# Performance work log

Measured on AMD Instinct MI355X. Metric: run time of the kernel, lower is better.

Reference implementation:

```python
import jax, jax.numpy as jnp
import numpy as np

C = 256; CM = 8; MAXI = 100; NCLS = 80
KP = (CM + 2) * CM + CM + CM * CM + CM + CM + 1  # 169 dynamic-kernel params

def _ln(x, g, b, eps=1e-5):
    m = x.mean(-1, keepdims=True)
    v = ((x - m) ** 2).mean(-1, keepdims=True)
    return g * (x - m) * jax.lax.rsqrt(v + eps) + b

def _mlp(x, hw, hb, lng, lnb, fw, fb):
    # torchvision MLP: [Linear -> LayerNorm -> SiLU] * n_hidden -> Linear
    for i in range(hw.shape[0]):
        x = jax.nn.silu(_ln(x @ hw[i] + hb[i], lng[i], lnb[i]))
    return x @ fw + fb

def _conv1x1_bn(x, w, s, b):
    # 1x1 conv (no bias) + inference-mode BatchNorm folded into per-channel affine
    y = jnp.einsum('bchw,oc->bohw', x, w)
    return y * s[None, :, None, None] + b[None, :, None, None]

def _grid(h, w):
    # normalized cell-center coordinates, (x, y) order, shape [h, w, 2]
    ys = (jnp.arange(h, dtype=jnp.float32) + 0.5) / h
    xs = (jnp.arange(w, dtype=jnp.float32) + 0.5) / w
    return jnp.stack([jnp.broadcast_to(xs[None, :], (h, w)),
                      jnp.broadcast_to(ys[:, None], (h, w))], axis=-1)

def setup_inputs() -> dict:
    key = jax.random.key(0)
    ks = iter(jax.random.split(key, 40))
    nrm = lambda shape, s=0.02: s * jax.random.normal(next(ks), shape, jnp.float32)
    B = 4
    inp = {
        'x0': jax.random.normal(next(ks), (B, 3, 512, 512), jnp.float32),
        'x1': jax.random.normal(next(ks), (B, 64, 256, 256), jnp.float32),
        'x2': jax.random.normal(next(ks), (B, 128, 128, 128), jnp.float32),
        'x3': jax.random.normal(next(ks), (B, 256, 64, 64), jnp.float32),
        'x4': jax.random.normal(next(ks), (B, 512, 32, 32), jnp.float32),
        'x5': jax.random.normal(next(ks), (B, 1024, 16, 16), jnp.float32),
        'lat3_w': nrm((C, 256)), 'lat3_s': jnp.ones((C,)), 'lat3_b': jnp.zeros((C,)),
        'lat4_w': nrm((C, 512)), 'lat4_s': jnp.ones((C,)), 'lat4_b': jnp.zeros((C,)),
        'lat5_w': nrm((C, 1024)), 'lat5_s': jnp.ones((C,)), 'lat5_b': jnp.zeros((C,)),
        'mlat_w': nrm((C, 256)), 'mlat_s': jnp.ones((C,)), 'mlat_b': jnp.zeros((C,)),
        'mhead_w': nrm((CM, C, 3, 3)), 'mhead_s': jnp.ones((CM,)), 'mhead_b': jnp.zeros((CM,)),
        'loc_hw': nrm((4, C, C)), 'loc_hb': jnp.zeros((4, C)), 'loc_lng': jnp.ones((4, C)), 'loc_lnb': jnp.zeros((4, C)),
        'loc_fw': nrm((C, 1)), 'loc_fb': -5.0 * jnp.ones((1,)),
        'cls_hw': nrm((4, C, C)), 'cls_hb': jnp.zeros((4, C)), 'cls_lng': jnp.ones((4, C)), 'cls_lnb': jnp.zeros((4, C)),
        'cls_fw': nrm((C, NCLS)), 'cls_fb': jnp.zeros((NCLS,)),
        'ker_hw': nrm((4, C, C)), 'ker_hb': jnp.zeros((4, C)), 'ker_lng': jnp.ones((4, C)), 'ker_lnb': jnp.zeros((4, C)),
        'ker_fw': nrm((C, KP)), 'ker_fb': jnp.zeros((KP,)),
    }
    return inp

def reference(x0, x1, x2, x3, x4, x5,
              lat3_w, lat3_s, lat3_b, lat4_w, lat4_s, lat4_b, lat5_w, lat5_s, lat5_b,
              mlat_w, mlat_s, mlat_b, mhead_w, mhead_s, mhead_b,
              loc_hw, loc_hb, loc_lng, loc_lnb, loc_fw, loc_fb,
              cls_hw, cls_hb, cls_lng, cls_lnb, cls_fw, cls_fb,
              ker_hw, ker_hb, ker_lng, ker_lnb, ker_fw, ker_fb):
    B, _, H, W = x0.shape
    lvls = [(x3, lat3_w, lat3_s, lat3_b), (x4, lat4_w, lat4_s, lat4_b), (x5, lat5_w, lat5_s, lat5_b)]
    feats = [_conv1x1_bn(x, w, s, b) for (x, w, s, b) in lvls]
    flat = jnp.concatenate([f.reshape(B, C, -1).transpose(0, 2, 1) for f in feats], axis=1)  # [B, L, C]
    loc_logits = _mlp(flat, loc_hw, loc_hb, loc_lng, loc_lnb, loc_fw, loc_fb)[..., 0]       # [B, L]
    top_vals, top_idx = jax.lax.top_k(loc_logits, MAXI)
    scores = jax.nn.sigmoid(top_vals)
    num_instances = (scores > 0.5).sum(axis=1)
    gfeat = jnp.take_along_axis(flat, top_idx[:, :, None], axis=1)  # [B, I, C]
    # mask branch
    mf = _conv1x1_bn(x3, mlat_w, mlat_s, mlat_b)
    mf = jax.lax.conv_general_dilated(mf, mhead_w, (1, 1), 'SAME', dimension_numbers=('NCHW', 'OIHW', 'NCHW'))
    mf = jax.nn.silu(mf * mhead_s[None, :, None, None] + mhead_b[None, :, None, None])  # [B, CM, h3, w3]
    h3, w3 = x3.shape[2], x3.shape[3]
    offs_flat = jnp.concatenate([_grid(x.shape[2], x.shape[3]).reshape(-1, 2) for x in (x3, x4, x5)], axis=0)
    offs = offs_flat[top_idx]                                # [B, I, 2]
    grid = _grid(h3, w3).transpose(2, 0, 1)                  # [2, h3, w3]
    grid = grid[None, None] - offs[:, :, :, None, None]      # [B, I, 2, h, w]
    mfi = jnp.broadcast_to(mf[:, None], (B, MAXI, CM, h3, w3))
    feats_i = jnp.concatenate([mfi, grid], axis=2)           # [B, I, CM+2, h, w]
    dyn = _mlp(gfeat, ker_hw, ker_hb, ker_lng, ker_lnb, ker_fw, ker_fb)  # [B, I, KP]
    c = CM
    o = (c + 2) * c
    w1 = dyn[..., :o].reshape(B, MAXI, c + 2, c)
    b1 = dyn[..., o:o + c].reshape(B, MAXI, c, 1, 1); o += c
    w2 = dyn[..., o:o + c * c].reshape(B, MAXI, c, c); o += c * c
    b2 = dyn[..., o:o + c].reshape(B, MAXI, c, 1, 1); o += c
    w3 = dyn[..., o:o + c].reshape(B, MAXI, c, 1); o += c
    b3 = dyn[..., o:].reshape(B, MAXI, 1, 1, 1)
    m = jax.nn.silu(jnp.einsum('bichw,bicd->bidhw', feats_i, w1) + b1)
    m = jax.nn.silu(jnp.einsum('bichw,bicd->bidhw', m, w2) + b2)
    m = jnp.einsum('bichw,bicd->bidhw', m, w3) + b3
    masks = jax.nn.sigmoid(m[:, :, 0])                       # [B, I, h3, w3]
    classes = jnp.argmax(_mlp(gfeat, cls_hw, cls_hb, cls_lng, cls_lnb, cls_fw, cls_fb), axis=-1)
    masks = jax.image.resize(masks, (B, MAXI, H, W), method='bilinear', antialias=False)
    return (num_instances, scores, classes, masks)
```

## Files before the change

kernel.cpp:

```cpp
#include <hip/hip_runtime.h>
#include <hip/hip_bf16.h>
#include <math.h>

#define DEVI __device__ __forceinline__

constexpr int LTOT  = 5376;
constexpr int NINST = 100;
constexpr int NCLS  = 80;
constexpr int KPAR  = 169;

DEVI float waveAllSum(float v) {
#pragma unroll
  for (int s = 32; s > 0; s >>= 1) v += __shfl_xor(v, s, 64);
  return v;
}
DEVI float siluf(float x) { return x / (1.0f + expf(-x)); }
DEVI float sigmf(float x) { return 1.0f / (1.0f + expf(-x)); }

__global__ __launch_bounds__(256) void wtrans(
    const float* __restrict__ w3, const float* __restrict__ w4,
    const float* __restrict__ w5, const float* __restrict__ wm,
    float* __restrict__ wt3, float* __restrict__ wt4,
    float* __restrict__ wt5, float* __restrict__ wtm)
{
  __shared__ float t[64][65];
  const int bid = blockIdx.x;
  const float* src; float* dst; int K, rel;
  if (bid < 16)       { src = w3; dst = wt3; K = 256;  rel = bid; }
  else if (bid < 48)  { src = w4; dst = wt4; K = 512;  rel = bid - 16; }
  else if (bid < 112) { src = w5; dst = wt5; K = 1024; rel = bid - 48; }
  else                { src = wm; dst = wtm; K = 256;  rel = bid - 112; }
  const int ctiles = K >> 6;
  const int ot = rel / ctiles, ct = rel % ctiles;
  const int o0 = ot * 64, c0 = ct * 64;
  const int tid = threadIdx.x;
#pragma unroll
  for (int s = 0; s < 16; ++s) {
    const int e = tid + 256*s;
    const int r = e >> 6, c = e & 63;
    t[r][c] = src[(long)(o0 + r)*K + c0 + c];
  }
  __syncthreads();
#pragma unroll
  for (int s = 0; s < 16; ++s) {
    const int e = tid + 256*s;
    const int q = e >> 6, p = e & 63;
    dst[(long)(c0 + q)*256 + o0 + p] = t[p][q];
  }
}

__global__ __launch_bounds__(256) void lateral_main(
    const float* __restrict__ x3, const float* __restrict__ x4, const float* __restrict__ x5,
    const float* __restrict__ wt3, const float* __restrict__ s3, const float* __restrict__ b3,
    const float* __restrict__ wt4, const float* __restrict__ s4, const float* __restrict__ b4,
    const float* __restrict__ wt5, const float* __restrict__ s5, const float* __restrict__ b5,
    const float* __restrict__ wtm, const float* __restrict__ sm, const float* __restrict__ bm,
    float* __restrict__ flat, float* __restrict__ mlatb)
{
  __shared__ float xs[32][36];
  __shared__ float ws[32][256];
  const int tid = threadIdx.x;
  const int rg = tid >> 6, cg = tid & 63;
  const int bid = blockIdx.x;
  const float *x, *wt, *sc, *bi;
  int K, P, b, p0, baseL = 0; bool tomlat = false;
  if (bid < 512)       { x=x3; wt=wt3; sc=s3; bi=b3; K=256;  P=4096; b=bid>>7;  p0=(bid&127)*32; }
  else if (bid < 1024) { const int rel=bid-512;  x=x3; wt=wtm; sc=sm; bi=bm; K=256;  P=4096; b=rel>>7; p0=(rel&127)*32; tomlat=true; }
  else if (bid < 1152) { const int rel=bid-1024; x=x4; wt=wt4; sc=s4; bi=b4; K=512;  P=1024; b=rel>>5; p0=(rel&31)*32; baseL=4096; }
  else                 { const int rel=bid-1152; x=x5; wt=wt5; sc=s5; bi=b5; K=1024; P=256;  b=rel>>3; p0=(rel&7)*32;  baseL=5120; }
  const float* xb = x + (long)b * K * P;
  float acc[8][4] = {};
  const int nkb = K >> 5;
  for (int kb = 0; kb < nkb; ++kb) {
    __syncthreads();
#pragma unroll
    for (int s = 0; s < 4; ++s) {
      const int e = tid + 256*s;
      const int kk = e >> 5, px = e & 31;
      xs[kk][px] = xb[(long)(kb*32 + kk)*P + p0 + px];
    }
    {
      const float4* w4p = reinterpret_cast<const float4*>(wt + (kb << 13));
#pragma unroll
      for (int q = 0; q < 8; ++q) {
        const int c = tid + (q << 8);
        *reinterpret_cast<float4*>(&ws[c >> 6][4*(c & 63)]) = w4p[c];
      }
    }
    __syncthreads();
#pragma unroll
    for (int kk = 0; kk < 32; ++kk) {
      const float4 a0 = *reinterpret_cast<const float4*>(&xs[kk][8*rg]);
      const float4 a1 = *reinterpret_cast<const float4*>(&xs[kk][8*rg+4]);
      const float ar[8] = {a0.x,a0.y,a0.z,a0.w,a1.x,a1.y,a1.z,a1.w};
      const float4 wv = *reinterpret_cast<const float4*>(&ws[kk][4*cg]);
#pragma unroll
      for (int i = 0; i < 8; ++i) {
        acc[i][0] += ar[i]*wv.x; acc[i][1] += ar[i]*wv.y;
        acc[i][2] += ar[i]*wv.z; acc[i][3] += ar[i]*wv.w;
      }
    }
  }
  const float4 sA = *reinterpret_cast<const float4*>(&sc[4*cg]);
  const float4 bA = *reinterpret_cast<const float4*>(&bi[4*cg]);
  if (!tomlat) {
#pragma unroll
    for (int i = 0; i < 8; ++i) {
      const float4 ov = { acc[i][0]*sA.x+bA.x, acc[i][1]*sA.y+bA.y,
                          acc[i][2]*sA.z+bA.z, acc[i][3]*sA.w+bA.w };
      *reinterpret_cast<float4*>(&flat[((long)b*LTOT + baseL + p0 + 8*rg + i)*256 + 4*cg]) = ov;
    }
  } else {
#pragma unroll
    for (int j = 0; j < 4; ++j) {
      const float sj = (&sA.x)[j], bj = (&bA.x)[j];
      const float4 o0 = { acc[0][j]*sj+bj, acc[1][j]*sj+bj, acc[2][j]*sj+bj, acc[3][j]*sj+bj };
      const float4 o1 = { acc[4][j]*sj+bj, acc[5][j]*sj+bj, acc[6][j]*sj+bj, acc[7][j]*sj+bj };
      float* mb = &mlatb[((long)b*256 + 4*cg + j)*4096 + p0 + 8*rg];
      *reinterpret_cast<float4*>(mb) = o0;
      *reinterpret_cast<float4*>(mb + 4) = o1;
    }
  }
}

__global__ __attribute__((amdgpu_waves_per_eu(3, 3))) __launch_bounds__(256)
void loc4(
    const float* __restrict__ in, const float* __restrict__ hw,
    const float* __restrict__ hb, const float* __restrict__ lng, const float* __restrict__ lnb,
    const float* __restrict__ fw, const float* __restrict__ fb, float* __restrict__ logits)
{
  __shared__ float xls[4][7][256];
  const int tid = threadIdx.x;
  const int rg = tid >> 6, cg = tid & 63;
  const int r0 = blockIdx.x * 28 + rg * 7;
  float* xw = &xls[rg][0][0];
#pragma unroll
  for (int i = 0; i < 7; ++i) {
    const float4 v = *reinterpret_cast<const float4*>(&in[(long)(r0 + i)*256 + 4*cg]);
    *reinterpret_cast<float4*>(&xw[i*256 + 4*cg]) = v;
  }
  const float4 fw4 = *reinterpret_cast<const float4*>(&fw[4*cg]);
  const float fbv = fb[0];

#define LOADG(W, A, g)                                                      \
  {                                                                         \
    const int kk4 = (g) << 2;                                               \
    W[0] = *reinterpret_cast<const float4*>(&w[(kk4 + 0) << 8]);            \
    W[1] = *reinterpret_cast<const float4*>(&w[(kk4 + 1) << 8]);            \
    W[2] = *reinterpret_cast<const float4*>(&w[(kk4 + 2) << 8]);            \
    W[3] = *reinterpret_cast<const float4*>(&w[(kk4 + 3) << 8]);            \
    _Pragma("unroll")                                                       \
    for (int r = 0; r < 7; ++r)                                             \
      A[r] = *reinterpret_cast<const float4*>(&xw[r*256 + kk4]);            \
  }
#define FMAG(W, A)                                                          \
  _Pragma("unroll")                                                         \
  for (int u = 0; u < 4; ++u) {                                             \
    _Pragma("unroll")                                                       \
    for (int r = 0; r < 7; ++r) {                                           \
      const float a = (&A[r].x)[u];                                         \
      acc[r][0] += a*W[u].x; acc[r][1] += a*W[u].y;                         \
      acc[r][2] += a*W[u].z; acc[r][3] += a*W[u].w;                         \
    }                                                                       \
  }

  for (int L = 0; L < 4; ++L) {
    const float* w = hw + L*65536 + 4*cg;
    float acc[7][4] = {};
    float4 wvA[4], wvB[4], avA[7], avB[7];
    LOADG(wvA, avA, 0)
    for (int g = 0; g < 64; g += 2) {
      LOADG(wvB, avB, g + 1)
      FMAG(wvA, avA)
      if (g + 2 < 64) LOADG(wvA, avA, g + 2)
      FMAG(wvB, avB)
    }
    const float4 hb4 = *reinterpret_cast<const float4*>(&hb[L*256 + 4*cg]);
    const float4 g4  = *reinterpret_cast<const float4*>(&lng[L*256 + 4*cg]);
    const float4 lb4 = *reinterpret_cast<const float4*>(&lnb[L*256 + 4*cg]);
#pragma unroll
    for (int r = 0; r < 7; ++r) {
      const float y0 = acc[r][0]+hb4.x, y1 = acc[r][1]+hb4.y;
      const float y2 = acc[r][2]+hb4.z, y3 = acc[r][3]+hb4.w;
      const float m = waveAllSum(y0+y1+y2+y3) * (1.0f/256.0f);
      const float d0=y0-m, d1=y1-m, d2=y2-m, d3=y3-m;
      const float var = waveAllSum(d0*d0+d1*d1+d2*d2+d3*d3) * (1.0f/256.0f);
      const float rs = rsqrtf(var + 1e-5f);
      const float o0 = siluf(g4.x*d0*rs + lb4.x);
      const float o1 = siluf(g4.y*d1*rs + lb4.y);
      const float o2 = siluf(g4.z*d2*rs + lb4.z);
      const float o3 = siluf(g4.w*d3*rs + lb4.w);
      if (L < 3) {
        const float4 ov = {o0, o1, o2, o3};
        *reinterpret_cast<float4*>(&xw[r*256 + 4*cg]) = ov;
      } else {
        float d = o0*fw4.x + o1*fw4.y + o2*fw4.z + o3*fw4.w;
        d = waveAllSum(d);
        if (cg == 0) logits[r0 + r] = d + fbv;
      }
    }
  }
#undef LOADG
#undef FMAG
}

__global__ __launch_bounds__(256) void topk_gather(
    const float* __restrict__ logits, const float* __restrict__ flat,
    int* __restrict__ topi, float* __restrict__ gfeat,
    float* __restrict__ dout)
{
  __shared__ float sv[LTOT];
  __shared__ float rv[4];
  __shared__ int   ri[4];
  __shared__ int   sidx[NINST];
  const int b = blockIdx.x, tid = threadIdx.x;
  for (int l = tid; l < LTOT; l += 256) sv[l] = logits[b*LTOT + l];
  __syncthreads();
  int cnt = 0;
  for (int t = 0; t < NINST; ++t) {
    float bv = -INFINITY; int bidx = 0x7fffffff;
    for (int l = tid; l < LTOT; l += 256) {
      const float v = sv[l];
      if (v > bv) { bv = v; bidx = l; }
    }
#pragma unroll
    for (int s = 32; s > 0; s >>= 1) {
      const float v2 = __shfl_xor(bv, s, 64);
      const int   i2 = __shfl_xor(bidx, s, 64);
      if (v2 > bv || (v2 == bv && i2 < bidx)) { bv = v2; bidx = i2; }
    }
    if ((tid & 63) == 0) { rv[tid >> 6] = bv; ri[tid >> 6] = bidx; }
    __syncthreads();
    if (tid == 0) {
      bv = rv[0]; bidx = ri[0];
#pragma unroll
      for (int q = 1; q < 4; ++q)
        if (rv[q] > bv || (rv[q] == bv && ri[q] < bidx)) { bv = rv[q]; bidx = ri[q]; }
      sidx[t] = bidx; topi[b*NINST + t] = bidx;
      dout[4 + b*NINST + t] = sigmf(bv);
      if (bv > 0.0f) ++cnt;
      sv[bidx] = -INFINITY;
    }
    __syncthreads();
  }
  if (tid == 0) dout[b] = (float)cnt;
  for (int t = 0; t < NINST; ++t) {
    const int ix = sidx[t];
    gfeat[((long)b*NINST + t)*256 + tid] = flat[((long)b*LTOT + ix)*256 + tid];
  }
}

__global__ __launch_bounds__(256) void clsker4(
    const float* __restrict__ gfeat, float* __restrict__ h2,
    const float* __restrict__ chw, const float* __restrict__ chb,
    const float* __restrict__ cg_, const float* __restrict__ cb_,
    const float* __restrict__ khw, const float* __restrict__ khb,
    const float* __restrict__ kg_, const float* __restrict__ kb_)
{
  __shared__ float xs[256][12];
  __shared__ float wsm[16][256];
  const int tid = threadIdx.x;
  const int rg = tid >> 6, cg = tid & 63;
  const bool ker = blockIdx.x >= 50;
  const int r0 = (ker ? (blockIdx.x - 50) : blockIdx.x) * 8;
  const int outr0 = r0 + (ker ? 400 : 0);
  const float* hw = ker ? khw : chw;
  const float* hb = ker ? khb : chb;
  const float* g_ = ker ? kg_ : cg_;
  const float* lb = ker ? kb_ : cb_;
#pragma unroll
  for (int s = 0; s < 2; ++s) {
    const int e = tid + 256*s;
    const int row = e >> 6, q = e & 63;
    const float4 v = *reinterpret_cast<const float4*>(&gfeat[(long)(r0 + row)*256 + 4*q]);
    const int pc = 2*((row >> 1) ^ (q & 3)) + (row & 1);
#pragma unroll
    for (int j = 0; j < 4; ++j) xs[4*q+j][pc] = (&v.x)[j];
  }
  float ov[2][4];
  for (int L = 0; L < 4; ++L) {
    const float* w = hw + L*65536;
    float acc[2][4] = {};
    for (int kb = 0; kb < 16; ++kb) {
      __syncthreads();
      const float4* w4 = reinterpret_cast<const float4*>(w + (kb << 12));
#pragma unroll
      for (int q = 0; q < 4; ++q) {
        const int c = tid + (q << 8);
        *reinterpret_cast<float4*>(&wsm[c>>6][4*(c&63)]) = w4[c];
      }
      __syncthreads();
#pragma unroll
      for (int kk = 0; kk < 16; ++kk) {
        const int k = (kb << 4) + kk;
        const float2 av = *reinterpret_cast<const float2*>(&xs[k][2*(rg ^ ((k >> 2) & 3))]);
        const float4 wv = *reinterpret_cast<const float4*>(&wsm[kk][4*cg]);
        acc[0][0] += av.x*wv.x; acc[0][1] += av.x*wv.y; acc[0][2] += av.x*wv.z; acc[0][3] += av.x*wv.w;
        acc[1][0] += av.y*wv.x; acc[1][1] += av.y*wv.y; acc[1][2] += av.y*wv.z; acc[1][3] += av.y*wv.w;
      }
    }
    const float4 hb4 = *reinterpret_cast<const float4*>(&hb[L*256 + 4*cg]);
    const float4 g4  = *reinterpret_cast<const float4*>(&g_[L*256 + 4*cg]);
    const float4 lb4 = *reinterpret_cast<const float4*>(&lb[L*256 + 4*cg]);
#pragma unroll
    for (int i = 0; i < 2; ++i) {
      const float y0 = acc[i][0]+hb4.x, y1 = acc[i][1]+hb4.y;
      const float y2 = acc[i][2]+hb4.z, y3 = acc[i][3]+hb4.w;
      const float m = waveAllSum(y0+y1+y2+y3) * (1.0f/256.0f);
      const float d0=y0-m, d1=y1-m, d2=y2-m, d3=y3-m;
      const float var = waveAllSum(d0*d0+d1*d1+d2*d2+d3*d3) * (1.0f/256.0f);
      const float rs = rsqrtf(var + 1e-5f);
      ov[i][0] = siluf(g4.x*d0*rs + lb4.x);
      ov[i][1] = siluf(g4.y*d1*rs + lb4.y);
      ov[i][2] = siluf(g4.z*d2*rs + lb4.z);
      ov[i][3] = siluf(g4.w*d3*rs + lb4.w);
    }
    __syncthreads();
    if (L < 3) {
      const int pc = 2*(rg ^ (cg & 3));
#pragma unroll
      for (int j = 0; j < 4; ++j) {
        const float2 t = {ov[0][j], ov[1][j]};
        *reinterpret_cast<float2*>(&xs[4*cg+j][pc]) = t;
      }
    }
  }
#pragma unroll
  for (int i = 0; i < 2; ++i) {
    const float4 o = {ov[i][0], ov[i][1], ov[i][2], ov[i][3]};
    *reinterpret_cast<float4*>(&h2[(long)(outr0 + 2*rg + i)*256 + 4*cg]) = o;
  }
}

__global__ __launch_bounds__(256) void heads(
    const float* __restrict__ h2, const float* __restrict__ cfw, const float* __restrict__ cfb,
    const float* __restrict__ kfw, const float* __restrict__ kfb,
    float* __restrict__ dout, float* __restrict__ dyn)
{
  __shared__ float xr[256];
  __shared__ float lv[NCLS];
  const int bid = blockIdx.x, tid = threadIdx.x;
  xr[tid] = h2[(long)bid*256 + tid];
  __syncthreads();
  if (bid < 400) {
    if (tid < NCLS) {
      float a0=0.f, a1=0.f, a2=0.f, a3=0.f;
      for (int k = 0; k < 256; k += 4) {
        a0 += xr[k+0]*cfw[(k+0)*NCLS + tid];
        a1 += xr[k+1]*cfw[(k+1)*NCLS + tid];
        a2 += xr[k+2]*cfw[(k+2)*NCLS + tid];
        a3 += xr[k+3]*cfw[(k+3)*NCLS + tid];
      }
      lv[tid] = (a0+a1) + (a2+a3) + cfb[tid];
    }
    __syncthreads();
    if (tid == 0) {
      float bv = lv[0]; int bi2 = 0;
      for (int o = 1; o < NCLS; ++o) if (lv[o] > bv) { bv = lv[o]; bi2 = o; }
      dout[404 + bid] = (float)bi2;
    }
  } else {
    if (tid < KPAR) {
      float a0=0.f, a1=0.f, a2=0.f, a3=0.f;
      for (int k = 0; k < 256; k += 4) {
        a0 += xr[k+0]*kfw[(k+0)*KPAR + tid];
        a1 += xr[k+1]*kfw[(k+1)*KPAR + tid];
        a2 += xr[k+2]*kfw[(k+2)*KPAR + tid];
        a3 += xr[k+3]*kfw[(k+3)*KPAR + tid];
      }
      dyn[(long)(bid-400)*KPAR + tid] = (a0+a1) + (a2+a3) + kfb[tid];
    }
  }
}

__global__ __launch_bounds__(256) void conv3(
    const float* __restrict__ mlat, const float* __restrict__ mw,
    float* __restrict__ partial)
{
  const int bid = blockIdx.x;
  const int cc = bid & 7;
  const int tile = (bid >> 3) & 15;
  const int b = bid >> 7;
  const int y0 = (tile >> 2)*16, x0 = (tile & 3)*16;
  const int tid = threadIdx.x;
  const int ly = tid >> 4, lx = tid & 15;
  __shared__ float til[2][18][19];
  __shared__ float wch[8][32][12];
  for (int e = tid; e < 2304; e += 256) {
    const int o = e / 288, rem = e % 288;
    const int c = rem / 9, qq = rem - c*9;
    wch[o][c][qq] = mw[((o*256) + cc*32 + c)*9 + qq];
  }
  int lofs[3], gofs[3], chn[3]; bool vld[3], has[3];
  float* tf = &til[0][0][0];
#pragma unroll
  for (int s = 0; s < 3; ++s) {
    const int e = tid + 256*s;
    has[s] = (e < 648);
    lofs[s] = 0; gofs[s] = 0; chn[s] = 0; vld[s] = false;
    if (has[s]) {
      const int ch = (e >= 324) ? 1 : 0;
      const int pos = e - ch*324;
      const int iy = pos / 18, ix = pos - iy*18;
      const int gy = y0 - 1 + iy, gx = x0 - 1 + ix;
      vld[s] = (gy >= 0 && gy < 64 && gx >= 0 && gx < 64);
      lofs[s] = ch*342 + iy*19 + ix;
      gofs[s] = gy*64 + gx;
      chn[s] = ch;
    }
  }
  const float* xbase = mlat + ((long)b*256 + cc*32)*4096;
  float acc[8] = {};
  for (int r = 0; r < 16; ++r) {
    __syncthreads();
#pragma unroll
    for (int s = 0; s < 3; ++s)
      if (has[s]) tf[lofs[s]] = vld[s] ? xbase[(long)(2*r + chn[s])*4096 + gofs[s]] : 0.f;
    __syncthreads();
#pragma unroll
    for (int ch = 0; ch < 2; ++ch) {
      const int c = 2*r + ch;
      float t[9];
#pragma unroll
      for (int dy = 0; dy < 3; ++dy)
#pragma unroll
        for (int dx = 0; dx < 3; ++dx) t[dy*3+dx] = til[ch][ly+dy][lx+dx];
#pragma unroll
      for (int o = 0; o < 8; ++o) {
        const float4 wa = *reinterpret_cast<const float4*>(&wch[o][c][0]);
        const float4 wb = *reinterpret_cast<const float4*>(&wch[o][c][4]);
        const float w8 = wch[o][c][8];
        acc[o] += t[0]*wa.x + t[1]*wa.y + t[2]*wa.z + t[3]*wa.w
                + t[4]*wb.x + t[5]*wb.y + t[6]*wb.z + t[7]*wb.w + t[8]*w8;
      }
    }
  }
  const long pbase = (((long)b*8 + cc)*8)*4096 + (y0+ly)*64 + (x0+lx);
#pragma unroll
  for (int o = 0; o < 8; ++o) partial[pbase + (long)o*4096] = acc[o];
}

__global__ __launch_bounds__(256) void mhead_fin(
    const float* __restrict__ partial, const float* __restrict__ s,
    const float* __restrict__ bi, float* __restrict__ mhead)
{
  const int idx = blockIdx.x*256 + threadIdx.x;
  const int p = idx & 4095;
  const int o = (idx >> 12) & 7;
  const int b = idx >> 15;
  float v = 0.f;
#pragma unroll
  for (int cc = 0; cc < 8; ++cc) v += partial[(((long)b*8 + cc)*8 + o)*4096 + p];
  v = v*s[o] + bi[o];
  mhead[idx] = siluf(v);
}

__global__ __launch_bounds__(256) void mask_fused(
    const float* __restrict__ dyn, const int* __restrict__ topi,
    const float* __restrict__ mhead, float* __restrict__ dout)
{
  __shared__ float msrc[18][64];
  __shared__ float dd[KPAR];
  __shared__ float so[2];
  const int bid = blockIdx.x;
  const int inst = bid >> 2, q = bid & 3;
  const int tid = threadIdx.x;
  if (tid < KPAR) dd[tid] = dyn[(long)inst*KPAR + tid];
  if (tid == 0) {
    const int l = topi[inst];
    float ox, oy;
    if (l < 4096)      { ox = ((l & 63) + 0.5f)*(1.f/64.f); oy = ((l >> 6) + 0.5f)*(1.f/64.f); }
    else if (l < 5120) { const int t = l - 4096; ox = ((t & 31) + 0.5f)*(1.f/32.f); oy = ((t >> 5) + 0.5f)*(1.f/32.f); }
    else               { const int t = l - 5120; ox = ((t & 15) + 0.5f)*(1.f/16.f); oy = ((t >> 4) + 0.5f)*(1.f/16.f); }
    so[0] = ox; so[1] = oy;
  }
  __syncthreads();
  const float ox = so[0], oy = so[1];
  const int b = inst / NINST;
  const float* mh = mhead + (long)b*8*4096;
  const int r0s = 16*q - 1;
  for (int e = tid; e < 1152; e += 256) {
    const int r = e >> 6, x = e & 63;
    int sy = r0s + r; sy = sy < 0 ? 0 : (sy > 63 ? 63 : sy);
    const int p = sy*64 + x;
    float f[10];
#pragma unroll
    for (int c = 0; c < 8; ++c) f[c] = mh[c*4096 + p];
    f[8] = (x + 0.5f)*(1.f/64.f) - ox;
    f[9] = (sy + 0.5f)*(1.f/64.f) - oy;
    float m1[8];
#pragma unroll
    for (int d = 0; d < 8; ++d) {
      float t = dd[80 + d];
#pragma unroll
      for (int c = 0; c < 10; ++c) t += f[c]*dd[c*8 + d];
      m1[d] = siluf(t);
    }
    float m2[8];
#pragma unroll
    for (int d = 0; d < 8; ++d) {
      float t = dd[152 + d];
#pragma unroll
      for (int c = 0; c < 8; ++c) t += m1[c]*dd[88 + c*8 + d];
      m2[d] = siluf(t);
    }
    float o = dd[168];
#pragma unroll
    for (int c = 0; c < 8; ++c) o += m2[c]*dd[160 + c];
    msrc[r][x] = sigmf(o);
  }
  __syncthreads();
  const int j4 = tid & 127;
  const int half = tid >> 7;
  const int ix0 = (j4 & 1) ? (j4 >> 1) : (j4 >> 1) - 1;
  const int xlo = ix0 < 0 ? 0 : ix0;
  const int xhi = (ix0 + 1 > 63) ? 63 : ix0 + 1;
  float fx[4];
#pragma unroll
  for (int m = 0; m < 4; ++m) {
    const int x = 4*j4 + m;
    const float tx = (x + 0.5f)*0.125f - 0.5f;
    fx[m] = tx - (float)ix0;
  }
  float* dbase = dout + 804 + ((long)inst << 18);
  for (int it = 0; it < 64; ++it) {
    const int yy = 2*it + half;
    const int y = 128*q + yy;
    const float ty = (y + 0.5f)*0.125f - 0.5f;
    const float fyf = floorf(ty);
    const int iy0 = (int)fyf;
    const float fy = ty - fyf;
    const int r0 = iy0 - r0s;
    const float L0 = msrc[r0][xlo],   R0 = msrc[r0][xhi];
    const float L1 = msrc[r0+1][xlo], R1 = msrc[r0+1][xhi];
    const float L = L0 + (L1 - L0)*fy;
    const float R = R0 + (R1 - R0)*fy;
    const float4 ovv = { L + (R - L)*fx[0], L + (R - L)*fx[1],
                         L + (R - L)*fx[2], L + (R - L)*fx[3] };
    *reinterpret_cast<float4*>(&dbase[((long)y << 9) + (j4 << 2)]) = ovv;
  }
}

extern "C" void kernel_launch(void* const* d_in, const int* in_sizes, int n_in,
                              void* d_out, int out_size, void* d_ws, size_t ws_size,
                              hipStream_t stream)
{
  (void)in_sizes; (void)n_in; (void)out_size; (void)ws_size;
  const float* x3      = (const float*)d_in[3];
  const float* x4      = (const float*)d_in[4];
  const float* x5      = (const float*)d_in[5];
  const float* lat3_w  = (const float*)d_in[6];
  const float* lat3_s  = (const float*)d_in[7];
  const float* lat3_b  = (const float*)d_in[8];
  const float* lat4_w  = (const float*)d_in[9];
  const float* lat4_s  = (const float*)d_in[10];
  const float* lat4_b  = (const float*)d_in[11];
  const float* lat5_w  = (const float*)d_in[12];
  const float* lat5_s  = (const float*)d_in[13];
  const float* lat5_b  = (const float*)d_in[14];
  const float* mlat_w  = (const float*)d_in[15];
  const float* mlat_s  = (const float*)d_in[16];
  const float* mlat_b  = (const float*)d_in[17];
  const float* mhead_w = (const float*)d_in[18];
  const float* mhead_s = (const float*)d_in[19];
  const float* mhead_b = (const float*)d_in[20];
  const float* loc_hw  = (const float*)d_in[21];
  const float* loc_hb  = (const float*)d_in[22];
  const float* loc_lng = (const float*)d_in[23];
  const float* loc_lnb = (const float*)d_in[24];
  const float* loc_fw  = (const float*)d_in[25];
  const float* loc_fb  = (const float*)d_in[26];
  const float* cls_hw  = (const float*)d_in[27];
  const float* cls_hb  = (const float*)d_in[28];
  const float* cls_lng = (const float*)d_in[29];
  const float* cls_lnb = (const float*)d_in[30];
  const float* cls_fw  = (const float*)d_in[31];
  const float* cls_fb  = (const float*)d_in[32];
  const float* ker_hw  = (const float*)d_in[33];
  const float* ker_hb  = (const float*)d_in[34];
  const float* ker_lng = (const float*)d_in[35];
  const float* ker_lnb = (const float*)d_in[36];
  const float* ker_fw  = (const float*)d_in[37];
  const float* ker_fb  = (const float*)d_in[38];

  float* ws      = (float*)d_ws;
  float* flat    = ws;
  float* mlatb   = ws + 5505024;
  float* partial = ws + 9699328;
  float* mheadb  = ws + 10747904;
  float* h2      = ws + 10878976;
  float* logits  = ws + 11083776;
  int*   topi    = (int*)(ws + 11105280);
  float* gfeat   = ws + 11105680;
  float* dynb    = ws + 11208080;
  float* wt3     = ws + 11275680;
  float* wt4     = ws + 11341216;
  float* wt5     = ws + 11472288;
  float* wtm     = ws + 11734432;
  float* dout    = (float*)d_out;

  wtrans<<<128, 256, 0, stream>>>(lat3_w, lat4_w, lat5_w, mlat_w, wt3, wt4, wt5, wtm);
  lateral_main<<<1184, 256, 0, stream>>>(x3, x4, x5,
      wt3, lat3_s, lat3_b, wt4, lat4_s, lat4_b, wt5, lat5_s, lat5_b,
      wtm, mlat_s, mlat_b, flat, mlatb);
  conv3<<<512, 256, 0, stream>>>(mlatb, mhead_w, partial);
  mhead_fin<<<512, 256, 0, stream>>>(partial, mhead_s, mhead_b, mheadb);
  loc4<<<768, 256, 0, stream>>>(flat, loc_hw, loc_hb, loc_lng, loc_lnb,
                                loc_fw, loc_fb, logits);
  topk_gather<<<4, 256, 0, stream>>>(logits, flat, topi, gfeat, dout);
  clsker4<<<100, 256, 0, stream>>>(gfeat, h2,
      cls_hw, cls_hb, cls_lng, cls_lnb, ker_hw, ker_hb, ker_lng, ker_lnb);
  heads<<<800, 256, 0, stream>>>(h2, cls_fw, cls_fb, ker_fw, ker_fb, dout, dynb);
  mask_fused<<<1600, 256, 0, stream>>>(dynb, topi, mheadb, dout);
}
```

Baseline: 782.6 us.

## Cache per-thread top-k maxima and drop shared weight staging in hidden MLP

In top-k selection, each thread keeps its local best value and index and rescans its strided slice only when its candidate won the round. Previously every thread rescanned all of shared memory on each of the 100 iterations. The hidden-MLP kernel no longer stages weight tiles through shared memory behind block barriers. Each wave now streams weights directly from global memory with a software double-buffered register pipeline, and keeps its own two rows in a per-wave LDS slice. This removes most __syncthreads, at the cost of redundant global weight reads across the four waves, which rely on L1/L2 hits.

```diff
diff --git a/kernel.cpp b/kernel.cpp
--- a/kernel.cpp
+++ b/kernel.cpp
@@ -213,16 +213,18 @@
   __shared__ float rv[4];
   __shared__ int   ri[4];
   __shared__ int   sidx[NINST];
+  __shared__ int   winsh;
   const int b = blockIdx.x, tid = threadIdx.x;
   for (int l = tid; l < LTOT; l += 256) sv[l] = logits[b*LTOT + l];
   __syncthreads();
+  float bvt = -INFINITY; int bit = 0x7fffffff;
+  for (int l = tid; l < LTOT; l += 256) {
+    const float v = sv[l];
+    if (v > bvt) { bvt = v; bit = l; }
+  }
   int cnt = 0;
   for (int t = 0; t < NINST; ++t) {
-    float bv = -INFINITY; int bidx = 0x7fffffff;
-    for (int l = tid; l < LTOT; l += 256) {
-      const float v = sv[l];
-      if (v > bv) { bv = v; bidx = l; }
-    }
+    float bv = bvt; int bidx = bit;
 #pragma unroll
     for (int s = 32; s > 0; s >>= 1) {
       const float v2 = __shfl_xor(bv, s, 64);
@@ -239,11 +241,21 @@
       sidx[t] = bidx; topi[b*NINST + t] = bidx;
       dout[4 + b*NINST + t] = sigmf(bv);
       if (bv > 0.0f) ++cnt;
-      sv[bidx] = -INFINITY;
+      winsh = bidx;
     }
     __syncthreads();
+    const int wi = winsh;
+    if (bit == wi) {
+      sv[wi] = -INFINITY;
+      bvt = -INFINITY; bit = 0x7fffffff;
+      for (int l = tid; l < LTOT; l += 256) {
+        const float v = sv[l];
+        if (v > bvt) { bvt = v; bit = l; }
+      }
+    }
   }
   if (tid == 0) dout[b] = (float)cnt;
+  __syncthreads();
   for (int t = 0; t < NINST; ++t) {
     const int ix = sidx[t];
     gfeat[((long)b*NINST + t)*256 + tid] = flat[((long)b*LTOT + ix)*256 + tid];
@@ -257,47 +269,55 @@
     const float* __restrict__ khw, const float* __restrict__ khb,
     const float* __restrict__ kg_, const float* __restrict__ kb_)
 {
-  __shared__ float xs[256][12];
-  __shared__ float wsm[16][256];
+  __shared__ float xls[4][2][256];
   const int tid = threadIdx.x;
   const int rg = tid >> 6, cg = tid & 63;
   const bool ker = blockIdx.x >= 50;
-  const int r0 = (ker ? (blockIdx.x - 50) : blockIdx.x) * 8;
-  const int outr0 = r0 + (ker ? 400 : 0);
+  const int rb = (ker ? (blockIdx.x - 50) : blockIdx.x) * 8;
+  const int r0 = rb + 2*rg;
+  const int ob = r0 + (ker ? 400 : 0);
   const float* hw = ker ? khw : chw;
   const float* hb = ker ? khb : chb;
   const float* g_ = ker ? kg_ : cg_;
   const float* lb = ker ? kb_ : cb_;
-#pragma unroll
-  for (int s = 0; s < 2; ++s) {
-    const int e = tid + 256*s;
-    const int row = e >> 6, q = e & 63;
-    const float4 v = *reinterpret_cast<const float4*>(&gfeat[(long)(r0 + row)*256 + 4*q]);
-    const int pc = 2*((row >> 1) ^ (q & 3)) + (row & 1);
-#pragma unroll
-    for (int j = 0; j < 4; ++j) xs[4*q+j][pc] = (&v.x)[j];
-  }
-  float ov[2][4];
+  float* xw = &xls[rg][0][0];
+#pragma unroll
+  for (int i = 0; i < 2; ++i) {
+    const float4 v = *reinterpret_cast<const float4*>(&gfeat[(long)(r0 + i)*256 + 4*cg]);
+    *reinterpret_cast<float4*>(&xw[i*256 + 4*cg]) = v;
+  }
+
+#define LOADG2(W, A, g)                                                     \
+  {                                                                         \
+    const int kk4 = (g) << 2;                                               \
+    W[0] = *reinterpret_cast<const float4*>(&w[(kk4 + 0) << 8]);            \
+    W[1] = *reinterpret_cast<const float4*>(&w[(kk4 + 1) << 8]);            \
+    W[2] = *reinterpret_cast<const float4*>(&w[(kk4 + 2) << 8]);            \
+    W[3] = *reinterpret_cast<const float4*>(&w[(kk4 + 3) << 8]);            \
+    A[0] = *reinterpret_cast<const float4*>(&xw[kk4]);                      \
+    A[1] = *reinterpret_cast<const float4*>(&xw[256 + kk4]);                \
+  }
+#define FMAG2(W, A)                                                         \
+  _Pragma("unroll")                                                         \
+  for (int u = 0; u < 4; ++u) {                                             \
+    _Pragma("unroll")                                                       \
+    for (int r = 0; r < 2; ++r) {                                           \
+      const float a = (&A[r].x)[u];                                         \
+      acc[r][0] += a*W[u].x; acc[r][1] += a*W[u].y;                         \
+      acc[r][2] += a*W[u].z; acc[r][3] += a*W[u].w;                         \
+    }                                                                       \
+  }
+
   for (int L = 0; L < 4; ++L) {
-    const float* w = hw + L*65536;
+    const float* w = hw + L*65536 + 4*cg;
     float acc[2][4] = {};
-    for (int kb = 0; kb < 16; ++kb) {
-      __syncthreads();
-      const float4* w4 = reinterpret_cast<const float4*>(w + (kb << 12));
-#pragma unroll
-      for (int q = 0; q < 4; ++q) {
-        const int c = tid + (q << 8);
-        *reinterpret_cast<float4*>(&wsm[c>>6][4*(c&63)]) = w4[c];
-      }
-      __syncthreads();
-#pragma unroll
-      for (int kk = 0; kk < 16; ++kk) {
-        const int k = (kb << 4) + kk;
-        const float2 av = *reinterpret_cast<const float2*>(&xs[k][2*(rg ^ ((k >> 2) & 3))]);
-        const float4 wv = *reinterpret_cast<const float4*>(&wsm[kk][4*cg]);
-        acc[0][0] += av.x*wv.x; acc[0][1] += av.x*wv.y; acc[0][2] += av.x*wv.z; acc[0][3] += av.x*wv.w;
-        acc[1][0] += av.y*wv.x; acc[1][1] += av.y*wv.y; acc[1][2] += av.y*wv.z; acc[1][3] += av.y*wv.w;
-      }
+    float4 wvA[4], wvB[4], avA[2], avB[2];
+    LOADG2(wvA, avA, 0)
+    for (int g = 0; g < 64; g += 2) {
+      LOADG2(wvB, avB, g + 1)
+      FMAG2(wvA, avA)
+      if (g + 2 < 64) LOADG2(wvA, avA, g + 2)
+      FMAG2(wvB, avB)
     }
     const float4 hb4 = *reinterpret_cast<const float4*>(&hb[L*256 + 4*cg]);
     const float4 g4  = *reinterpret_cast<const float4*>(&g_[L*256 + 4*cg]);
@@ -310,26 +330,14 @@
       const float d0=y0-m, d1=y1-m, d2=y2-m, d3=y3-m;
       const float var = waveAllSum(d0*d0+d1*d1+d2*d2+d3*d3) * (1.0f/256.0f);
       const float rs = rsqrtf(var + 1e-5f);
-      ov[i][0] = siluf(g4.x*d0*rs + lb4.x);
-      ov[i][1] = siluf(g4.y*d1*rs + lb4.y);
-      ov[i][2] = siluf(g4.z*d2*rs + lb4.z);
-      ov[i][3] = siluf(g4.w*d3*rs + lb4.w);
-    }
-    __syncthreads();
-    if (L < 3) {
-      const int pc = 2*(rg ^ (cg & 3));
-#pragma unroll
-      for (int j = 0; j < 4; ++j) {
-        const float2 t = {ov[0][j], ov[1][j]};
-        *reinterpret_cast<float2*>(&xs[4*cg+j][pc]) = t;
-      }
-    }
-  }
-#pragma unroll
-  for (int i = 0; i < 2; ++i) {
-    const float4 o = {ov[i][0], ov[i][1], ov[i][2], ov[i][3]};
-    *reinterpret_cast<float4*>(&h2[(long)(outr0 + 2*rg + i)*256 + 4*cg]) = o;
-  }
+      const float4 ov = { siluf(g4.x*d0*rs + lb4.x), siluf(g4.y*d1*rs + lb4.y),
+                          siluf(g4.z*d2*rs + lb4.z), siluf(g4.w*d3*rs + lb4.w) };
+      if (L < 3) *reinterpret_cast<float4*>(&xw[i*256 + 4*cg]) = ov;
+      else       *reinterpret_cast<float4*>(&h2[(long)(ob + i)*256 + 4*cg]) = ov;
+    }
+  }
+#undef LOADG2
+#undef FMAG2
 }
 
 __global__ __launch_bounds__(256) void heads(
```

Result: no change. 793.0 us (+1.3%).
